# Kernel tuning notes

Measured on AMD Instinct MI355X. Metric: run time of the kernel, lower is better.

The kernel has to match this reference:

```python
import jax, jax.numpy as jnp
import numpy as np

NEG = 0.01  # leaky_relu negative slope used throughout AttentiveFP


def _seg_softmax(logits, seg, num):
    # softmax over entries grouped by segment id (PyG softmax w/ 1e-16 eps)
    m = jax.ops.segment_max(logits, seg, num_segments=num)
    m = jnp.where(jnp.isfinite(m), m, 0.0)
    e = jnp.exp(logits - m[seg])
    s = jax.ops.segment_sum(e, seg, num_segments=num)
    return e / (s[seg] + 1e-16)


def _gru(x, h, wi, wh, bi, bh):
    # torch.nn.GRUCell math
    gi = x @ wi.T + bi
    gh = h @ wh.T + bh
    ir, iz, inn = jnp.split(gi, 3, axis=-1)
    hr, hz, hn = jnp.split(gh, 3, axis=-1)
    r = jax.nn.sigmoid(ir + hr)
    z = jax.nn.sigmoid(iz + hz)
    n = jnp.tanh(inn + r * hn)
    return (1.0 - z) * n + z * h


def _forward(x, edge_attr, mol_feats, lin1_w, lin1_b, gate_lin1_w, gate_lin2_w, gate_att_l, gate_att_r, gate_bias, grus_wi, grus_wh, grus_bi, grus_bh, atom_w, atom_att_src, atom_att_dst, atom_bias, mol_w, mol_att_src, mol_att_dst, mol_bias, lin2_w, lin2_b, fcm0_w, fcm0_b, fcm1_w, fcm1_b, fcm2_w, fcm2_b, fc0_w, fc0_b, fc1_w, fc1_b, fc2_w, fc2_b, fc3_w, fc3_b, fc4_w, fc4_b, edge_index, batch):
    N = x.shape[0]
    G = mol_feats.shape[0]
    src, dst = edge_index[0], edge_index[1]
    lrelu = lambda v: jax.nn.leaky_relu(v, NEG)
    # AttentiveFP (eval mode: dropout off)
    xh = lrelu(x @ lin1_w.T + lin1_b)  # [N,H]
    # --- GATEConv: edge-conditioned attention, add aggregation ---
    m = lrelu(jnp.concatenate([xh[src], edge_attr], axis=-1) @ gate_lin1_w.T)  # [E,H]
    a = lrelu(m @ gate_att_l + (xh @ gate_att_r)[dst])
    a = _seg_softmax(a, dst, N)
    h = jax.ops.segment_sum((m @ gate_lin2_w.T) * a[:, None], dst, num_segments=N) + gate_bias
    xh = jax.nn.relu(_gru(jax.nn.elu(h), xh, grus_wi[0], grus_wh[0], grus_bi[0], grus_bh[0]))
    # --- GATConv layers (num_layers-1 = 2, heads=1, no self loops) ---
    for l in range(2):
        xl = xh @ atom_w[l].T
        a = lrelu((xl @ atom_att_src[l])[src] + (xl @ atom_att_dst[l])[dst])
        a = _seg_softmax(a, dst, N)
        h = jax.ops.segment_sum(xl[src] * a[:, None], dst, num_segments=N) + atom_bias[l]
        xh = jax.nn.relu(_gru(jax.nn.elu(h), xh, grus_wi[1 + l], grus_wh[1 + l], grus_bi[1 + l], grus_bh[1 + l]))
    # --- attentive graph readout (num_timesteps = 3) ---
    out = jax.nn.relu(jax.ops.segment_sum(xh, batch, num_segments=G))  # [G,H]
    xm = xh @ mol_w.T            # atom-side lin (x fixed across timesteps)
    a_src = xm @ mol_att_src
    for _ in range(3):
        a = lrelu(a_src + ((out @ mol_w.T) @ mol_att_dst)[batch])
        a = _seg_softmax(a, batch, G)
        h = jax.ops.segment_sum(xm * a[:, None], batch, num_segments=G) + mol_bias
        out = jax.nn.relu(_gru(jax.nn.elu(h), out, grus_wi[3], grus_wh[3], grus_bi[3], grus_bh[3]))
    hg = out @ lin2_w.T + lin2_b  # [G,256]
    # --- mol-feature MLP branch (SiLU) ---
    hm = jax.nn.silu(mol_feats @ fcm0_w.T + fcm0_b)
    hm = jax.nn.silu(hm @ fcm1_w.T + fcm1_b)
    hm = jax.nn.silu(hm @ fcm2_w.T + fcm2_b)
    # --- fusion MLP ---
    hg = jnp.concatenate([hg, hm], axis=1)  # [G,512]
    hg = jax.nn.silu(hg @ fc0_w.T + fc0_b)
    hg = jax.nn.silu(hg @ fc1_w.T + fc1_b)
    hg = jax.nn.silu(hg @ fc2_w.T + fc2_b)
    hg = jax.nn.silu(hg @ fc3_w.T + fc3_b)
    return hg @ fc4_w.T + fc4_b  # [G,1]


def setup_inputs() -> dict:
    key = jax.random.key(0)
    ks = iter(jax.random.split(key, 64))
    def W(*shape):
        return jax.random.normal(next(ks), shape, jnp.float32) / np.float32(np.sqrt(shape[-1]))
    def B(*shape):
        return 0.02 * jax.random.normal(next(ks), shape, jnp.float32)
    N, E, G = 131072, 262144, 8192
    Fn, Fe, Fm, H = 64, 16, 200, 256
    return dict(
        x=jax.random.normal(next(ks), (N, Fn), jnp.float32),
        edge_attr=jax.random.normal(next(ks), (E, Fe), jnp.float32),
        mol_feats=jax.random.normal(next(ks), (G, Fm), jnp.float32),
        lin1_w=W(H, Fn), lin1_b=B(H),
        gate_lin1_w=W(H, H + Fe), gate_lin2_w=W(H, H),
        gate_att_l=W(H), gate_att_r=W(H), gate_bias=B(H),
        grus_wi=W(4, 3 * H, H), grus_wh=W(4, 3 * H, H), grus_bi=B(4, 3 * H), grus_bh=B(4, 3 * H),
        atom_w=W(2, H, H), atom_att_src=W(2, H), atom_att_dst=W(2, H), atom_bias=B(2, H),
        mol_w=W(H, H), mol_att_src=W(H), mol_att_dst=W(H), mol_bias=B(H),
        lin2_w=W(H, H), lin2_b=B(H),
        fcm0_w=W(H, Fm), fcm0_b=B(H), fcm1_w=W(H, H), fcm1_b=B(H), fcm2_w=W(H, H), fcm2_b=B(H),
        fc0_w=W(512, 512), fc0_b=B(512), fc1_w=W(512, 512), fc1_b=B(512),
        fc2_w=W(512, 512), fc2_b=B(512), fc3_w=W(128, 512), fc3_b=B(128),
        fc4_w=W(1, 128), fc4_b=B(1),
        edge_index=jax.random.randint(next(ks), (2, E), 0, N),
        batch=jnp.sort(jax.random.randint(next(ks), (N,), 0, G)),
    )


def reference(x, edge_attr, mol_feats, lin1_w, lin1_b, gate_lin1_w, gate_lin2_w, gate_att_l, gate_att_r, gate_bias, grus_wi, grus_wh, grus_bi, grus_bh, atom_w, atom_att_src, atom_att_dst, atom_bias, mol_w, mol_att_src, mol_att_dst, mol_bias, lin2_w, lin2_b, fcm0_w, fcm0_b, fcm1_w, fcm1_b, fcm2_w, fcm2_b, fc0_w, fc0_b, fc1_w, fc1_b, fc2_w, fc2_b, fc3_w, fc3_b, fc4_w, fc4_b, edge_index, batch):
    return _forward(x, edge_attr, mol_feats, lin1_w, lin1_b, gate_lin1_w, gate_lin2_w, gate_att_l, gate_att_r, gate_bias, grus_wi, grus_wh, grus_bi, grus_bh, atom_w, atom_att_src, atom_att_dst, atom_bias, mol_w, mol_att_src, mol_att_dst, mol_bias, lin2_w, lin2_b, fcm0_w, fcm0_b, fcm1_w, fcm1_b, fcm2_w, fcm2_b, fc0_w, fc0_b, fc1_w, fc1_b, fc2_w, fc2_b, fc3_w, fc3_b, fc4_w, fc4_b, edge_index, batch)
```

## Files before the change

kernel.cpp:

```cpp
#include <hip/hip_runtime.h>
#include <hip/hip_bf16.h>
#include <math.h>


typedef unsigned short u16;
typedef u16 u16x8 __attribute__((ext_vector_type(8)));
typedef short s16x8 __attribute__((ext_vector_type(8)));
typedef float f32x4 __attribute__((ext_vector_type(4)));

__device__ __forceinline__ float u2f(u16 u) { return __uint_as_float(((unsigned)u) << 16); }
__device__ __forceinline__ u16 f2u(float f) {
    return __builtin_bit_cast(u16, __float2bfloat16(f));
}

#define NEGS 0.01f

__device__ __forceinline__ unsigned fkey(float f) {
    unsigned u = __float_as_uint(f);
    return (u & 0x80000000u) ? ~u : (u | 0x80000000u);
}
__device__ __forceinline__ float funkey(unsigned k) {
    return (k & 0x80000000u) ? __uint_as_float(k ^ 0x80000000u) : __uint_as_float(~k);
}
#define KEY_NEG_INF 0x007FFFFFu

static inline int cdiv(int a, int b) { return (a + b - 1) / b; }

__global__ void fill_f32(float* p, float v, size_t n) {
    size_t i = (size_t)blockIdx.x * 256 + threadIdx.x;
    if (i < n) p[i] = v;
}
__global__ void fill_u32(unsigned* p, unsigned v, int n) {
    int i = blockIdx.x * 256 + threadIdx.x;
    if (i < n) p[i] = v;
}
__global__ void relu_inplace(float* p, size_t n) {
    size_t i = (size_t)blockIdx.x * 256 + threadIdx.x;
    if (i < n) p[i] = fmaxf(p[i], 0.f);
}
__global__ void copy_f2b(const float* s, u16* d, size_t n) {
    size_t i = (size_t)blockIdx.x * 256 + threadIdx.x;
    if (i < n) d[i] = f2u(s[i]);
}
__global__ void copy_ff(const float* s, float* d, size_t n) {
    size_t i = (size_t)blockIdx.x * 256 + threadIdx.x;
    if (i < n) d[i] = s[i];
}
__global__ void matvecT_k(const float* W, const float* a, float* v, int K, int Jout) {
    int j = blockIdx.x * 256 + threadIdx.x;
    if (j >= Jout) return;
    float s = 0.f;
    for (int k = 0; k < K; k++) s += W[(size_t)k * Jout + j] * a[k];
    v[j] = s;
}
__global__ void edge_add_lrelu(float* elog, const float* r, const int* dsti, int E) {
    int i = blockIdx.x * 256 + threadIdx.x;
    if (i < E) {
        float v = elog[i] + r[dsti[i]];
        elog[i] = v > 0.f ? v : NEGS * v;
    }
}
__global__ void pair_logit(float* elog, const float* s, const float* d,
                           const int* srci, const int* dsti, int E) {
    int i = blockIdx.x * 256 + threadIdx.x;
    if (i < E) {
        float v = s[srci[i]] + d[dsti[i]];
        elog[i] = v > 0.f ? v : NEGS * v;
    }
}
__global__ void node_logit(float* nlog, const float* asrc, const float* wg,
                           const int* batch, int N) {
    int i = blockIdx.x * 256 + threadIdx.x;
    if (i < N) {
        float v = asrc[i] + wg[batch[i]];
        nlog[i] = v > 0.f ? v : NEGS * v;
    }
}
__global__ void seg_max_k(const float* logit, const int* idx, unsigned* key, int n) {
    int i = blockIdx.x * 256 + threadIdx.x;
    if (i < n) atomicMax(&key[idx[i]], fkey(logit[i]));
}
__global__ void seg_exp_k(const float* logit, const int* idx, const unsigned* key,
                          float* ex, float* sum, int n) {
    int i = blockIdx.x * 256 + threadIdx.x;
    if (i < n) {
        float e = expf(logit[i] - funkey(key[idx[i]]));
        ex[i] = e;
        atomicAdd(&sum[idx[i]], e);
    }
}
__global__ void seg_div_k(const float* ex, const int* idx, const float* sum,
                          float* a, int n) {
    int i = blockIdx.x * 256 + threadIdx.x;
    if (i < n) a[i] = ex[i] / (sum[idx[i]] + 1e-16f);
}
__global__ void scatter_rows_b(const u16* V, const int* gsrc, const float* sc,
                               const int* gdst, float* dst, int M) {
    int r = blockIdx.x;
    if (r >= M) return;
    int c = threadIdx.x;
    int vr = gsrc ? gsrc[r] : r;
    float v = u2f(V[(size_t)vr * 256 + c]);
    if (sc) v *= sc[r];
    atomicAdd(&dst[(size_t)gdst[r] * 256 + c], v);
}
__global__ void rowdot2_b(const u16* X, const float* v1, const float* v2,
                          float* o1, float* o2, int M) {
    int r = blockIdx.x * 4 + (threadIdx.x >> 6);
    int lane = threadIdx.x & 63;
    if (r >= M) return;
    const u16* row = X + (size_t)r * 256 + lane * 4;
    float p1 = 0.f, p2 = 0.f;
#pragma unroll
    for (int q = 0; q < 4; q++) {
        float xv = u2f(row[q]);
        p1 += xv * v1[lane * 4 + q];
        if (v2) p2 += xv * v2[lane * 4 + q];
    }
    for (int off = 32; off; off >>= 1) {
        p1 += __shfl_down(p1, off);
        if (v2) p2 += __shfl_down(p2, off);
    }
    if (lane == 0) {
        o1[r] = p1;
        if (v2) o2[r] = p2;
    }
}
__global__ void rowdot_f(const float* X, const float* v1, float* o1, int M) {
    int r = blockIdx.x * 4 + (threadIdx.x >> 6);
    int lane = threadIdx.x & 63;
    if (r >= M) return;
    float4 a = ((const float4*)(X + (size_t)r * 256))[lane];
    float4 b = ((const float4*)v1)[lane];
    float p1 = a.x * b.x + a.y * b.y + a.z * b.z + a.w * b.w;
    for (int off = 32; off; off >>= 1) p1 += __shfl_down(p1, off);
    if (lane == 0) o1[r] = p1;
}
__global__ void fc4_k(const float* X, const float* w, const float* b, float* out, int G) {
    int g = blockIdx.x * 4 + (threadIdx.x >> 6);
    int lane = threadIdx.x & 63;
    if (g >= G) return;
    float2 xv = ((const float2*)(X + (size_t)g * 128))[lane];
    float2 wv = ((const float2*)w)[lane];
    float p = xv.x * wv.x + xv.y * wv.y;
    for (int off = 32; off; off >>= 1) p += __shfl_down(p, off);
    if (lane == 0) out[g] = p + b[0];
}

__global__ void pack_w(const float* s1, const float* s2, int K1, int Ksrc,
                       int Nout, int Kp, u16* dst) {
    int idx = blockIdx.x * 256 + threadIdx.x;
    int kiters = Kp >> 5;
    int total = (Nout >> 7) * kiters * 512;
    if (idx >= total) return;
    int c = idx & 511;
    int rest = idx >> 9;
    int ki = rest % kiters, nb = rest / kiters;
    int n = (nb << 7) + (((c >> 6) & 7) << 4) + (c & 15);
    int k0 = (ki << 5) + (((c >> 4) & 3) << 3);
    u16x8 vh, vl;
#pragma unroll
    for (int j = 0; j < 8; j++) {
        int k = k0 + j;
        float f = 0.f;
        if (k < K1) f = s1[(size_t)n * K1 + k];
        else if (k < Ksrc) f = s2[(size_t)n * (Ksrc - K1) + (k - K1)];
        u16 h = f2u(f);
        vh[j] = h;
        vl[j] = f2u(f - u2f(h));
    }
    ((u16x8*)dst)[idx] = vh;
    ((u16x8*)dst)[idx + total] = vl;
}
__global__ void pack_gru_w(const float* wi, const float* wh, u16* dst) {
    int idx = blockIdx.x * 256 + threadIdx.x;
    const int total = 8 * 16 * 512;
    if (idx >= total) return;
    int c = idx & 511, rest = idx >> 9;
    int ki = rest & 15, nb = rest >> 4;
    int n = (nb << 7) + (((c >> 6) & 7) << 4) + (c & 15);
    int k0 = (ki << 5) + (((c >> 4) & 3) << 3);
    int grp = n >> 6, sub = (n >> 4) & 3, ch = grp * 16 + (n & 15);
    u16x8 vh, vl;
#pragma unroll
    for (int j = 0; j < 8; j++) {
        int k = k0 + j;
        float f;
        if (sub < 3) {
            int srow = sub * 256 + ch;
            f = (k < 256) ? wi[(size_t)srow * 256 + k]
                          : wh[(size_t)srow * 256 + (k - 256)];
        } else {
            f = (k < 256) ? 0.f : wh[(size_t)(512 + ch) * 256 + (k - 256)];
        }
        u16 h = f2u(f);
        vh[j] = h;
        vl[j] = f2u(f - u2f(h));
    }
    ((u16x8*)dst)[idx] = vh;
    ((u16x8*)dst)[idx + total] = vl;
}
__global__ void pack_gru_b(const float* bi, const float* bh, float* bp) {
    int n = blockIdx.x * 256 + threadIdx.x;
    if (n >= 1024) return;
    int grp = n >> 6, sub = (n >> 4) & 3, ch = grp * 16 + (n & 15);
    float v;
    if (sub == 0) v = bi[ch] + bh[ch];
    else if (sub == 1) v = bi[256 + ch] + bh[256 + ch];
    else if (sub == 2) v = bi[512 + ch] + bh[512 + ch];
    else v = bh[512 + ch];
    bp[n] = v;
}

struct p8 { u16x8 hi, lo; };
__device__ __forceinline__ u16x8 zero8() {
    u16x8 z;
#pragma unroll
    for (int j = 0; j < 8; j++) z[j] = 0;
    return z;
}
__device__ __forceinline__ p8 sp_zero() { p8 r; r.hi = zero8(); r.lo = zero8(); return r; }
__device__ __forceinline__ p8 sp_b(const u16* p) {
    p8 r;
    r.hi = *(const u16x8*)p;
    r.lo = zero8();
    return r;
}
__device__ __forceinline__ p8 sp_f(const float* p) {
    p8 r;
#pragma unroll
    for (int j = 0; j < 8; j++) {
        float x = p[j];
        u16 h = f2u(x);
        r.hi[j] = h;
        r.lo[j] = f2u(x - u2f(h));
    }
    return r;
}
__device__ __forceinline__ p8 sp_eluf(const float* p) {
    p8 r;
#pragma unroll
    for (int j = 0; j < 8; j++) {
        float x = p[j];
        float e = x > 0.f ? x : expm1f(x);
        u16 h = f2u(e);
        r.hi[j] = h;
        r.lo[j] = f2u(e - u2f(h));
    }
    return r;
}
template <int ALD>
__device__ __forceinline__ p8 ldA(bool valid, int k, int Ksrc, const u16* ab,
                                  const float* af, const float* x2) {
    if (!valid) return sp_zero();
    if (ALD == 1) {
        if (k >= Ksrc) return sp_zero();
        return sp_f(af + k);
    }
    if (ALD == 2) {
        if (k < 256) return sp_b(ab + k);
        if (k < 272) return sp_f(x2 + (k - 256));
        return sp_zero();
    }
    if (ALD == 3) {
        if (k < 256) return sp_eluf(af + k);
        return sp_b(ab + (k - 256));
    }
    if (k < 256) return sp_eluf(af + k);
    return sp_f(x2 + (k - 256));
}
template <int ALD>
__device__ __forceinline__ bool lo_zero(int ki) {
    if (ALD == 2) return ki < 8;
    if (ALD == 3) return ki >= 8;
    return false;
}
template <int ACT>
__device__ __forceinline__ float actf(float v) {
    if (ACT == 1) return v > 0.f ? v : NEGS * v;
    if (ACT == 3) return v / (1.f + expf(-v));
    return v;
}

template <int ALD, int ACT, int EPI>
__global__ __launch_bounds__(256, 2) void mgemm(
    int M, int Kp, int Ksrc,
    const float* Af, int lda, const u16* Ab,
    const int* gidx, const float* X2f, const u16* Wp,
    const float* b1,
    float* Cf, u16* Cb, int ldc,
    const float* attv, float* dotout,
    const int* didx, const float* escale, float* scat) {
    __shared__ u16x8 lsAh[512];
    __shared__ u16x8 lsAl[512];
    __shared__ u16x8 lsWh[512];
    __shared__ u16x8 lsWl[512];
    const int t = threadIdx.x;
    const int m0 = blockIdx.x * 128;
    const int nb = blockIdx.y;
    const int kiters = Kp >> 5;
    const int r0 = ((t >> 6) << 4) | (t & 15);
    const int kq = ((t >> 4) & 3) << 3;
    const int mA[2] = {m0 + r0, m0 + r0 + 64};
    const u16* abr[2];
    const float* afr[2];
    const float* x2r[2];
    bool val[2];
#pragma unroll
    for (int h = 0; h < 2; h++) {
        int m = mA[h];
        val[h] = (m < M);
        int ms = val[h] ? m : 0;
        abr[h] = nullptr; afr[h] = nullptr; x2r[h] = nullptr;
        if (ALD == 1) {
            afr[h] = Af + (size_t)ms * lda;
        } else if (ALD == 2) {
            abr[h] = Ab + (size_t)gidx[ms] * 256;
            x2r[h] = X2f + (size_t)ms * 16;
        } else if (ALD == 3) {
            afr[h] = Af + (size_t)ms * 256;
            abr[h] = Ab + (size_t)ms * 256;
        } else {
            afr[h] = Af + (size_t)ms * 256;
            x2r[h] = X2f + (size_t)ms * 256;
        }
    }
    const int wave = t >> 6, lane = t & 63;
    const int wm = (wave >> 1) << 6, wn = (wave & 1) << 6;
    f32x4 acc[4][4];
#pragma unroll
    for (int i = 0; i < 4; i++)
#pragma unroll
        for (int j = 0; j < 4; j++) {
            acc[i][j][0] = 0.f; acc[i][j][1] = 0.f; acc[i][j][2] = 0.f; acc[i][j][3] = 0.f;
        }
    const u16x8* wh0 = (const u16x8*)Wp + ((size_t)nb * kiters << 9);
    const u16x8* wl0 = wh0 + ((size_t)gridDim.y * kiters << 9);
    for (int ki = 0; ki < kiters; ki++) {
        int kb = (ki << 5) + kq;
        p8 a0 = ldA<ALD>(val[0], kb, Ksrc, abr[0], afr[0], x2r[0]);
        p8 a1 = ldA<ALD>(val[1], kb, Ksrc, abr[1], afr[1], x2r[1]);
        lsAh[t] = a0.hi; lsAl[t] = a0.lo;
        lsAh[t + 256] = a1.hi; lsAl[t + 256] = a1.lo;
        const u16x8* wsh = wh0 + ((size_t)ki << 9);
        const u16x8* wsl = wl0 + ((size_t)ki << 9);
        lsWh[t] = wsh[t]; lsWh[t + 256] = wsh[t + 256];
        lsWl[t] = wsl[t]; lsWl[t + 256] = wsl[t + 256];
        __syncthreads();
        s16x8 ah[4], al[4], wh[4], wl[4];
#pragma unroll
        for (int f = 0; f < 4; f++) {
            int ai = ((wm >> 4) + f) * 64 + lane;
            int wi = ((wn >> 4) + f) * 64 + lane;
            ah[f] = __builtin_bit_cast(s16x8, lsAh[ai]);
            al[f] = __builtin_bit_cast(s16x8, lsAl[ai]);
            wh[f] = __builtin_bit_cast(s16x8, lsWh[wi]);
            wl[f] = __builtin_bit_cast(s16x8, lsWl[wi]);
        }
        bool skip_lh = lo_zero<ALD>(ki);
#pragma unroll
        for (int fi = 0; fi < 4; fi++)
#pragma unroll
            for (int fj = 0; fj < 4; fj++) {
                acc[fi][fj] = __builtin_amdgcn_mfma_f32_16x16x32_bf16(
                    ah[fi], wh[fj], acc[fi][fj], 0, 0, 0);
                if (!skip_lh)
                    acc[fi][fj] = __builtin_amdgcn_mfma_f32_16x16x32_bf16(
                        al[fi], wh[fj], acc[fi][fj], 0, 0, 0);
                acc[fi][fj] = __builtin_amdgcn_mfma_f32_16x16x32_bf16(
                    ah[fi], wl[fj], acc[fi][fj], 0, 0, 0);
            }
        __syncthreads();
    }
    const int col = lane & 15, quad = lane >> 4;
    const int n_base = nb * 128 + wn;
    if (EPI == 2) {
        float dp[4][4] = {};
#pragma unroll
        for (int fi = 0; fi < 4; fi++)
#pragma unroll
            for (int fj = 0; fj < 4; fj++) {
                int nn = n_base + fj * 16 + col;
                float av = attv[nn];
#pragma unroll
                for (int r = 0; r < 4; r++) dp[fi][r] += actf<ACT>(acc[fi][fj][r]) * av;
            }
#pragma unroll
        for (int fi = 0; fi < 4; fi++)
#pragma unroll
            for (int r = 0; r < 4; r++) {
                float p = dp[fi][r];
                p += __shfl_down(p, 8);
                p += __shfl_down(p, 4);
                p += __shfl_down(p, 2);
                p += __shfl_down(p, 1);
                int mm = m0 + wm + fi * 16 + quad * 4 + r;
                if (col == 0 && mm < M) atomicAdd(dotout + mm, p);
            }
    } else if (EPI == 3) {
#pragma unroll
        for (int fi = 0; fi < 4; fi++)
#pragma unroll
            for (int r = 0; r < 4; r++) {
                int mm = m0 + wm + fi * 16 + quad * 4 + r;
                if (mm >= M) continue;
                int d = didx[mm];
                float s = escale[mm];
                float* rowp = scat + (size_t)d * 256;
#pragma unroll
                for (int fj = 0; fj < 4; fj++) {
                    int nn = n_base + fj * 16 + col;
                    atomicAdd(rowp + nn, actf<ACT>(acc[fi][fj][r]) * s);
                }
            }
    } else {
#pragma unroll
        for (int fj = 0; fj < 4; fj++) {
            int nn = n_base + fj * 16 + col;
            float bb = b1 ? b1[nn] : 0.f;
#pragma unroll
            for (int fi = 0; fi < 4; fi++)
#pragma unroll
                for (int r = 0; r < 4; r++) {
                    int mm = m0 + wm + fi * 16 + quad * 4 + r;
                    if (mm >= M) continue;
                    float v = actf<ACT>(acc[fi][fj][r] + bb);
                    if (EPI == 1) Cb[(size_t)mm * ldc + nn] = f2u(v);
                    else Cf[(size_t)mm * ldc + nn] = v;
                }
        }
    }
}

template <int ALD, bool HB>
__global__ __launch_bounds__(256, 2) void mgemm_gru(
    int M,
    const float* Af, const u16* Ab, const float* X2f,
    const u16* Wp, const float* bp,
    const u16* hb, const float* hf, float* of) {
    __shared__ u16x8 lsAh[512];
    __shared__ u16x8 lsAl[512];
    __shared__ u16x8 lsWh[512];
    __shared__ u16x8 lsWl[512];
    const int t = threadIdx.x;
    const int m0 = blockIdx.x * 128;
    const int nb = blockIdx.y;
    const int r0 = ((t >> 6) << 4) | (t & 15);
    const int kq = ((t >> 4) & 3) << 3;
    const int mA[2] = {m0 + r0, m0 + r0 + 64};
    const u16* abr[2];
    const float* afr[2];
    const float* x2r[2];
    bool val[2];
#pragma unroll
    for (int h = 0; h < 2; h++) {
        int m = mA[h];
        val[h] = (m < M);
        int ms = val[h] ? m : 0;
        abr[h] = nullptr; x2r[h] = nullptr;
        afr[h] = Af + (size_t)ms * 256;
        if (ALD == 3) abr[h] = Ab + (size_t)ms * 256;
        else x2r[h] = X2f + (size_t)ms * 256;
    }
    const int wave = t >> 6, lane = t & 63;
    const int wm = (wave >> 1) << 6, wn = (wave & 1) << 6;
    f32x4 acc[4][4];
#pragma unroll
    for (int i = 0; i < 4; i++)
#pragma unroll
        for (int j = 0; j < 4; j++) {
            acc[i][j][0] = 0.f; acc[i][j][1] = 0.f; acc[i][j][2] = 0.f; acc[i][j][3] = 0.f;
        }
    const u16x8* wh0 = (const u16x8*)Wp + ((size_t)nb * 16 << 9);
    const u16x8* wl0 = (const u16x8*)Wp + (size_t)(8 * 16 * 512) + ((size_t)nb * 16 << 9);
    for (int ki = 0; ki < 16; ki++) {
        int kb = (ki << 5) + kq;
        p8 a0 = ldA<ALD>(val[0], kb, 512, abr[0], afr[0], x2r[0]);
        p8 a1 = ldA<ALD>(val[1], kb, 512, abr[1], afr[1], x2r[1]);
        lsAh[t] = a0.hi; lsAl[t] = a0.lo;
        lsAh[t + 256] = a1.hi; lsAl[t + 256] = a1.lo;
        const u16x8* wsh = wh0 + ((size_t)ki << 9);
        const u16x8* wsl = wl0 + ((size_t)ki << 9);
        lsWh[t] = wsh[t]; lsWh[t + 256] = wsh[t + 256];
        lsWl[t] = wsl[t]; lsWl[t + 256] = wsl[t + 256];
        __syncthreads();
        s16x8 ah[4], al[4], wh[4], wl[4];
#pragma unroll
        for (int f = 0; f < 4; f++) {
            int ai = ((wm >> 4) + f) * 64 + lane;
            int wi = ((wn >> 4) + f) * 64 + lane;
            ah[f] = __builtin_bit_cast(s16x8, lsAh[ai]);
            al[f] = __builtin_bit_cast(s16x8, lsAl[ai]);
            wh[f] = __builtin_bit_cast(s16x8, lsWh[wi]);
            wl[f] = __builtin_bit_cast(s16x8, lsWl[wi]);
        }
        bool skip_lh = lo_zero<ALD>(ki);
        bool hn_zero = (ki < 8);
#pragma unroll
        for (int fi = 0; fi < 4; fi++)
#pragma unroll
            for (int fj = 0; fj < 4; fj++) {
                if (fj == 3 && hn_zero) continue;
                acc[fi][fj] = __builtin_amdgcn_mfma_f32_16x16x32_bf16(
                    ah[fi], wh[fj], acc[fi][fj], 0, 0, 0);
                if (!skip_lh)
                    acc[fi][fj] = __builtin_amdgcn_mfma_f32_16x16x32_bf16(
                        al[fi], wh[fj], acc[fi][fj], 0, 0, 0);
                acc[fi][fj] = __builtin_amdgcn_mfma_f32_16x16x32_bf16(
                    ah[fi], wl[fj], acc[fi][fj], 0, 0, 0);
            }
        __syncthreads();
    }
    const int col = lane & 15, quad = lane >> 4;
    const int nbase = nb * 128 + wn;
    float br = bp[nbase + col];
    float bz = bp[nbase + 16 + col];
    float bn = bp[nbase + 32 + col];
    float bhn = bp[nbase + 48 + col];
    int ch = (nb * 2 + (wn >> 6)) * 16 + col;
#pragma unroll
    for (int fi = 0; fi < 4; fi++)
#pragma unroll
        for (int r = 0; r < 4; r++) {
            int m = m0 + wm + fi * 16 + quad * 4 + r;
            if (m >= M) continue;
            float rs = acc[fi][0][r] + br;
            float zs = acc[fi][1][r] + bz;
            float nsv = acc[fi][2][r] + bn;
            float hnv = acc[fi][3][r] + bhn;
            float rr = 1.f / (1.f + expf(-rs));
            float zz = 1.f / (1.f + expf(-zs));
            float nn = tanhf(nsv - hnv + rr * hnv);
            float ho = HB ? u2f(hb[(size_t)m * 256 + ch]) : hf[(size_t)m * 256 + ch];
            of[(size_t)m * 256 + ch] = fmaxf((1.f - zz) * nn + zz * ho, 0.f);
        }
}

extern "C" void kernel_launch(void* const* d_in, const int* in_sizes, int n_in,
                              void* d_out, int out_size, void* d_ws, size_t ws_size,
                              hipStream_t stream) {
    const float* x = (const float*)d_in[0];
    const float* edge_attr = (const float*)d_in[1];
    const float* mol_feats = (const float*)d_in[2];
    const float* lin1_w = (const float*)d_in[3];
    const float* lin1_b = (const float*)d_in[4];
    const float* gate_lin1_w = (const float*)d_in[5];
    const float* gate_lin2_w = (const float*)d_in[6];
    const float* gate_att_l = (const float*)d_in[7];
    const float* gate_att_r = (const float*)d_in[8];
    const float* gate_bias = (const float*)d_in[9];
    const float* grus_wi = (const float*)d_in[10];
    const float* grus_wh = (const float*)d_in[11];
    const float* grus_bi = (const float*)d_in[12];
    const float* grus_bh = (const float*)d_in[13];
    const float* atom_w = (const float*)d_in[14];
    const float* atom_att_src = (const float*)d_in[15];
    const float* atom_att_dst = (const float*)d_in[16];
    const float* atom_bias = (const float*)d_in[17];
    const float* mol_w = (const float*)d_in[18];
    const float* mol_att_src = (const float*)d_in[19];
    const float* mol_att_dst = (const float*)d_in[20];
    const float* mol_bias = (const float*)d_in[21];
    const float* lin2_w = (const float*)d_in[22];
    const float* lin2_b = (const float*)d_in[23];
    const float* fcm0_w = (const float*)d_in[24];
    const float* fcm0_b = (const float*)d_in[25];
    const float* fcm1_w = (const float*)d_in[26];
    const float* fcm1_b = (const float*)d_in[27];
    const float* fcm2_w = (const float*)d_in[28];
    const float* fcm2_b = (const float*)d_in[29];
    const float* fc0_w = (const float*)d_in[30];
    const float* fc0_b = (const float*)d_in[31];
    const float* fc1_w = (const float*)d_in[32];
    const float* fc1_b = (const float*)d_in[33];
    const float* fc2_w = (const float*)d_in[34];
    const float* fc2_b = (const float*)d_in[35];
    const float* fc3_w = (const float*)d_in[36];
    const float* fc3_b = (const float*)d_in[37];
    const float* fc4_w = (const float*)d_in[38];
    const float* fc4_b = (const float*)d_in[39];
    const int* edge_index = (const int*)d_in[40];
    const int* batch = (const int*)d_in[41];
    float* out_final = (float*)d_out;

    const int N = in_sizes[0] / 64;
    const int E = in_sizes[1] / 16;
    const int G = in_sizes[2] / 200;
    const int* srcE = edge_index;
    const int* dstE = edge_index + E;

    char* base = (char*)d_ws;
    size_t off = 0;
    auto alloc = [&](size_t bytes) -> char* {
        char* p = base + off;
        off += (bytes + 255) & ~(size_t)255;
        return p;
    };
    u16* xh = (u16*)alloc((size_t)N * 256 * 2);
    float* hagg = (float*)alloc((size_t)N * 256 * 4);
    float* outg = (float*)alloc((size_t)G * 256 * 4);
    float* hgr = (float*)alloc((size_t)G * 256 * 4);
    float* elog = (float*)alloc((size_t)E * 4);
    float* eexp = (float*)alloc((size_t)E * 4);
    float* aedge = (float*)alloc((size_t)E * 4);
    unsigned* nkey = (unsigned*)alloc((size_t)N * 4);
    float* nsum = (float*)alloc((size_t)N * 4);
    float* ns1 = (float*)alloc((size_t)N * 4);
    float* ns2 = (float*)alloc((size_t)N * 4);
    unsigned* gkey = (unsigned*)alloc((size_t)G * 4);
    float* gsum = (float*)alloc((size_t)G * 4);
    float* wgb = (float*)alloc((size_t)G * 4);
    float* vbuf = (float*)alloc(1024 * 4);
    u16* pk_lin1 = (u16*)alloc(256 * 64 * 2 * 2);
    u16* pk_g1 = (u16*)alloc(256 * 288 * 2 * 2);
    u16* pk_g2 = (u16*)alloc(256 * 256 * 2 * 2);
    u16* pk_gruF[4];
    float* bp_gru[4];
    for (int l = 0; l < 4; l++) {
        pk_gruF[l] = (u16*)alloc(1024 * 512 * 2 * 2);
        bp_gru[l] = (float*)alloc(1024 * 4);
    }
    u16* pk_atom[2];
    for (int l = 0; l < 2; l++) pk_atom[l] = (u16*)alloc(256 * 256 * 2 * 2);
    u16* pk_mol = (u16*)alloc(256 * 256 * 2 * 2);
    u16* pk_lin2 = (u16*)alloc(256 * 256 * 2 * 2);
    u16* pk_fcm0 = (u16*)alloc(256 * 224 * 2 * 2);
    u16* pk_fcm1 = (u16*)alloc(256 * 256 * 2 * 2);
    u16* pk_fcm2 = (u16*)alloc(256 * 256 * 2 * 2);
    u16* pk_fc0 = (u16*)alloc(512 * 512 * 2 * 2);
    u16* pk_fc1 = (u16*)alloc(512 * 512 * 2 * 2);
    u16* pk_fc2 = (u16*)alloc(512 * 512 * 2 * 2);
    u16* pk_fc3 = (u16*)alloc(128 * 512 * 2 * 2);
    size_t fixed_bytes = off;
    if (fixed_bytes + (size_t)2 * 1024 * 1024 > ws_size) {
        fill_f32<<<cdiv(out_size, 256), 256, 0, stream>>>(out_final, (float)ws_size,
                                                          (size_t)out_size);
        return;
    }
    size_t avail = ws_size - fixed_bytes;
    float* cbuf = (float*)(base + fixed_bytes);
    int Mc = (int)((avail / 1024) & ~(size_t)127);
    if (Mc > N) Mc = N;
    if (Mc < 128) Mc = 128;
    float* fbufA = hagg;
    float* fbufB = fbufA + (size_t)G * 512;
    float* fbufC = fbufB + (size_t)G * 512;
    float* f128 = fbufC + (size_t)G * 512;
    float* hm1 = f128 + (size_t)G * 128;
    float* hm2 = hm1 + (size_t)G * 256;

    auto pack = [&](const float* s1, const float* s2, int K1, int Ksrc, int Nout,
                    int Kp, u16* dst) {
        int total = (Nout >> 7) * (Kp >> 5) * 512;
        pack_w<<<cdiv(total, 256), 256, 0, stream>>>(s1, s2, K1, Ksrc, Nout, Kp, dst);
    };
    pack(lin1_w, nullptr, 64, 64, 256, 64, pk_lin1);
    pack(gate_lin1_w, nullptr, 272, 272, 256, 288, pk_g1);
    pack(gate_lin2_w, nullptr, 256, 256, 256, 256, pk_g2);
    for (int l = 0; l < 4; l++) {
        pack_gru_w<<<cdiv(8 * 16 * 512, 256), 256, 0, stream>>>(
            grus_wi + (size_t)l * 768 * 256, grus_wh + (size_t)l * 768 * 256,
            pk_gruF[l]);
        pack_gru_b<<<4, 256, 0, stream>>>(grus_bi + (size_t)l * 768,
                                          grus_bh + (size_t)l * 768, bp_gru[l]);
    }
    for (int l = 0; l < 2; l++)
        pack(atom_w + (size_t)l * 256 * 256, nullptr, 256, 256, 256, 256, pk_atom[l]);
    pack(mol_w, nullptr, 256, 256, 256, 256, pk_mol);
    pack(lin2_w, nullptr, 256, 256, 256, 256, pk_lin2);
    pack(fcm0_w, nullptr, 200, 200, 256, 224, pk_fcm0);
    pack(fcm1_w, nullptr, 256, 256, 256, 256, pk_fcm1);
    pack(fcm2_w, nullptr, 256, 256, 256, 256, pk_fcm2);
    pack(fc0_w, nullptr, 512, 512, 512, 512, pk_fc0);
    pack(fc1_w, nullptr, 512, 512, 512, 512, pk_fc1);
    pack(fc2_w, nullptr, 512, 512, 512, 512, pk_fc2);
    pack(fc3_w, nullptr, 512, 512, 128, 512, pk_fc3);

#define NIL nullptr, nullptr, nullptr, nullptr, nullptr

    auto node_gru = [&](int l, const u16* Wpre, const float* bpre) {
        for (int c0 = 0; c0 < N; c0 += Mc) {
            int Ms = N - c0 < Mc ? N - c0 : Mc;
            int gx = cdiv(Ms, 128);
            mgemm<1, 0, 0><<<dim3(gx, 2), 256, 0, stream>>>(Ms, 256, 256,
                hagg + (size_t)c0 * 256, 256, nullptr, nullptr, nullptr,
                Wpre, bpre, cbuf, nullptr, 256, NIL);
            mgemm_gru<3, true><<<dim3(gx, 8), 256, 0, stream>>>(Ms,
                cbuf, xh + (size_t)c0 * 256, nullptr, pk_gruF[l], bp_gru[l],
                xh + (size_t)c0 * 256, nullptr, hagg + (size_t)c0 * 256);
        }
        copy_f2b<<<(int)(((size_t)N * 256 + 255) / 256), 256, 0, stream>>>(
            hagg, xh, (size_t)N * 256);
    };

    mgemm<1, 1, 1><<<dim3(cdiv(N, 128), 2), 256, 0, stream>>>(N, 64, 64,
        x, 64, nullptr, nullptr, nullptr, pk_lin1, lin1_b,
        nullptr, xh, 256, NIL);

    fill_f32<<<cdiv(E, 256), 256, 0, stream>>>(elog, 0.f, (size_t)E);
    mgemm<2, 1, 2><<<dim3(cdiv(E, 128), 2), 256, 0, stream>>>(E, 288, 272,
        nullptr, 0, xh, srcE, edge_attr, pk_g1, nullptr,
        nullptr, nullptr, 0, gate_att_l, elog, nullptr, nullptr, nullptr);
    rowdot2_b<<<cdiv(N, 4), 256, 0, stream>>>(xh, gate_att_r, nullptr, ns1, nullptr, N);
    edge_add_lrelu<<<cdiv(E, 256), 256, 0, stream>>>(elog, ns1, dstE, E);
    fill_u32<<<cdiv(N, 256), 256, 0, stream>>>(nkey, KEY_NEG_INF, N);
    fill_f32<<<cdiv(N, 256), 256, 0, stream>>>(nsum, 0.f, (size_t)N);
    seg_max_k<<<cdiv(E, 256), 256, 0, stream>>>(elog, dstE, nkey, E);
    seg_exp_k<<<cdiv(E, 256), 256, 0, stream>>>(elog, dstE, nkey, eexp, nsum, E);
    seg_div_k<<<cdiv(E, 256), 256, 0, stream>>>(eexp, dstE, nsum, aedge, E);
    fill_f32<<<(int)(((size_t)N * 256 + 255) / 256), 256, 0, stream>>>(
        hagg, 0.f, (size_t)N * 256);
    mgemm<2, 1, 3><<<dim3(cdiv(E, 128), 2), 256, 0, stream>>>(E, 288, 272,
        nullptr, 0, xh, srcE, edge_attr, pk_g1, nullptr,
        nullptr, nullptr, 0, nullptr, nullptr, dstE, aedge, hagg);
    node_gru(0, pk_g2, gate_bias);

    for (int l = 0; l < 2; l++) {
        const float* aw = atom_w + (size_t)l * 256 * 256;
        matvecT_k<<<1, 256, 0, stream>>>(aw, atom_att_src + (size_t)l * 256, vbuf, 256, 256);
        matvecT_k<<<1, 256, 0, stream>>>(aw, atom_att_dst + (size_t)l * 256, vbuf + 256, 256, 256);
        rowdot2_b<<<cdiv(N, 4), 256, 0, stream>>>(xh, vbuf, vbuf + 256, ns1, ns2, N);
        pair_logit<<<cdiv(E, 256), 256, 0, stream>>>(elog, ns1, ns2, srcE, dstE, E);
        fill_u32<<<cdiv(N, 256), 256, 0, stream>>>(nkey, KEY_NEG_INF, N);
        fill_f32<<<cdiv(N, 256), 256, 0, stream>>>(nsum, 0.f, (size_t)N);
        seg_max_k<<<cdiv(E, 256), 256, 0, stream>>>(elog, dstE, nkey, E);
        seg_exp_k<<<cdiv(E, 256), 256, 0, stream>>>(elog, dstE, nkey, eexp, nsum, E);
        seg_div_k<<<cdiv(E, 256), 256, 0, stream>>>(eexp, dstE, nsum, aedge, E);
        fill_f32<<<(int)(((size_t)N * 256 + 255) / 256), 256, 0, stream>>>(
            hagg, 0.f, (size_t)N * 256);
        scatter_rows_b<<<E, 256, 0, stream>>>(xh, srcE, aedge, dstE, hagg, E);
        node_gru(1 + l, pk_atom[l], atom_bias + (size_t)l * 256);
    }

    fill_f32<<<(int)(((size_t)G * 256 + 255) / 256), 256, 0, stream>>>(
        outg, 0.f, (size_t)G * 256);
    scatter_rows_b<<<N, 256, 0, stream>>>(xh, nullptr, nullptr, batch, outg, N);
    relu_inplace<<<(int)(((size_t)G * 256 + 255) / 256), 256, 0, stream>>>(
        outg, (size_t)G * 256);
    matvecT_k<<<1, 256, 0, stream>>>(mol_w, mol_att_dst, vbuf, 256, 256);
    matvecT_k<<<1, 256, 0, stream>>>(mol_w, mol_att_src, vbuf + 256, 256, 256);
    rowdot2_b<<<cdiv(N, 4), 256, 0, stream>>>(xh, vbuf + 256, nullptr, ns1, nullptr, N);
    int McG = Mc < G ? Mc : G;
    for (int t = 0; t < 3; t++) {
        rowdot_f<<<cdiv(G, 4), 256, 0, stream>>>(outg, vbuf, wgb, G);
        node_logit<<<cdiv(N, 256), 256, 0, stream>>>(elog, ns1, wgb, batch, N);
        fill_u32<<<cdiv(G, 256), 256, 0, stream>>>(gkey, KEY_NEG_INF, G);
        fill_f32<<<cdiv(G, 256), 256, 0, stream>>>(gsum, 0.f, (size_t)G);
        seg_max_k<<<cdiv(N, 256), 256, 0, stream>>>(elog, batch, gkey, N);
        seg_exp_k<<<cdiv(N, 256), 256, 0, stream>>>(elog, batch, gkey, eexp, gsum, N);
        seg_div_k<<<cdiv(N, 256), 256, 0, stream>>>(eexp, batch, gsum, aedge, N);
        fill_f32<<<(int)(((size_t)G * 256 + 255) / 256), 256, 0, stream>>>(
            hgr, 0.f, (size_t)G * 256);
        scatter_rows_b<<<N, 256, 0, stream>>>(xh, nullptr, aedge, batch, hgr, N);
        for (int c0 = 0; c0 < G; c0 += McG) {
            int Ms = G - c0 < McG ? G - c0 : McG;
            int gx = cdiv(Ms, 128);
            mgemm<1, 0, 0><<<dim3(gx, 2), 256, 0, stream>>>(Ms, 256, 256,
                hgr + (size_t)c0 * 256, 256, nullptr, nullptr, nullptr,
                pk_mol, mol_bias, cbuf, nullptr, 256, NIL);
            mgemm_gru<4, false><<<dim3(gx, 8), 256, 0, stream>>>(Ms,
                cbuf, nullptr, outg + (size_t)c0 * 256, pk_gruF[3], bp_gru[3],
                nullptr, outg + (size_t)c0 * 256, hgr + (size_t)c0 * 256);
        }
        copy_ff<<<(int)(((size_t)G * 256 + 255) / 256), 256, 0, stream>>>(
            hgr, outg, (size_t)G * 256);
    }

    int gG = cdiv(G, 128);
    mgemm<1, 0, 0><<<dim3(gG, 2), 256, 0, stream>>>(G, 256, 256, outg, 256,
        nullptr, nullptr, nullptr, pk_lin2, lin2_b,
        fbufA, nullptr, 512, NIL);
    mgemm<1, 3, 0><<<dim3(gG, 2), 256, 0, stream>>>(G, 224, 200, mol_feats, 200,
        nullptr, nullptr, nullptr, pk_fcm0, fcm0_b,
        hm1, nullptr, 256, NIL);
    mgemm<1, 3, 0><<<dim3(gG, 2), 256, 0, stream>>>(G, 256, 256, hm1, 256,
        nullptr, nullptr, nullptr, pk_fcm1, fcm1_b,
        hm2, nullptr, 256, NIL);
    mgemm<1, 3, 0><<<dim3(gG, 2), 256, 0, stream>>>(G, 256, 256, hm2, 256,
        nullptr, nullptr, nullptr, pk_fcm2, fcm2_b,
        fbufA + 256, nullptr, 512, NIL);
    mgemm<1, 3, 0><<<dim3(gG, 4), 256, 0, stream>>>(G, 512, 512, fbufA, 512,
        nullptr, nullptr, nullptr, pk_fc0, fc0_b,
        fbufB, nullptr, 512, NIL);
    mgemm<1, 3, 0><<<dim3(gG, 4), 256, 0, stream>>>(G, 512, 512, fbufB, 512,
        nullptr, nullptr, nullptr, pk_fc1, fc1_b,
        fbufC, nullptr, 512, NIL);
    mgemm<1, 3, 0><<<dim3(gG, 4), 256, 0, stream>>>(G, 512, 512, fbufC, 512,
        nullptr, nullptr, nullptr, pk_fc2, fc2_b,
        fbufB, nullptr, 512, NIL);
    mgemm<1, 3, 0><<<dim3(gG, 1), 256, 0, stream>>>(G, 512, 512, fbufB, 512,
        nullptr, nullptr, nullptr, pk_fc3, fc3_b,
        f128, nullptr, 128, NIL);
    fc4_k<<<cdiv(G, 4), 256, 0, stream>>>(f128, fc4_w, fc4_b, out_final, G);
}
```

Before: 6.628 ms.

## Replace atomic scatter aggregation with CSR gather and sorted segment reductions

```diff
diff --git a/kernel.cpp b/kernel.cpp
--- a/kernel.cpp
+++ b/kernel.cpp
@@ -34,17 +34,9 @@
     int i = blockIdx.x * 256 + threadIdx.x;
     if (i < n) p[i] = v;
 }
-__global__ void relu_inplace(float* p, size_t n) {
-    size_t i = (size_t)blockIdx.x * 256 + threadIdx.x;
-    if (i < n) p[i] = fmaxf(p[i], 0.f);
-}
 __global__ void copy_f2b(const float* s, u16* d, size_t n) {
     size_t i = (size_t)blockIdx.x * 256 + threadIdx.x;
     if (i < n) d[i] = f2u(s[i]);
-}
-__global__ void copy_ff(const float* s, float* d, size_t n) {
-    size_t i = (size_t)blockIdx.x * 256 + threadIdx.x;
-    if (i < n) d[i] = s[i];
 }
 __global__ void matvecT_k(const float* W, const float* a, float* v, int K, int Jout) {
     int j = blockIdx.x * 256 + threadIdx.x;
@@ -93,16 +85,6 @@
                           float* a, int n) {
     int i = blockIdx.x * 256 + threadIdx.x;
     if (i < n) a[i] = ex[i] / (sum[idx[i]] + 1e-16f);
-}
-__global__ void scatter_rows_b(const u16* V, const int* gsrc, const float* sc,
-                               const int* gdst, float* dst, int M) {
-    int r = blockIdx.x;
-    if (r >= M) return;
-    int c = threadIdx.x;
-    int vr = gsrc ? gsrc[r] : r;
-    float v = u2f(V[(size_t)vr * 256 + c]);
-    if (sc) v *= sc[r];
-    atomicAdd(&dst[(size_t)gdst[r] * 256 + c], v);
 }
 __global__ void rowdot2_b(const u16* X, const float* v1, const float* v2,
                           float* o1, float* o2, int M) {
@@ -145,6 +127,63 @@
     float p = xv.x * wv.x + xv.y * wv.y;
     for (int off = 32; off; off >>= 1) p += __shfl_down(p, off);
     if (lane == 0) out[g] = p + b[0];
+}
+
+__global__ void count_dst(const int* dst, int* cnt, int E) {
+    int i = blockIdx.x * 256 + threadIdx.x;
+    if (i < E) atomicAdd(&cnt[dst[i]], 1);
+}
+__global__ void alloc_rows(const int* cnt, int* rowstart, int* cursor, int N) {
+    int i = blockIdx.x * 256 + threadIdx.x;
+    if (i < N) rowstart[i] = atomicAdd(cursor, cnt[i]);
+}
+__global__ void fill_csr(const int* dst, const int* rowstart, int* fillc,
+                         int* eorder, int E) {
+    int e = blockIdx.x * 256 + threadIdx.x;
+    if (e >= E) return;
+    int d = dst[e];
+    int s = rowstart[d] + atomicAdd(&fillc[d], 1);
+    eorder[s] = e;
+}
+template <int MODE>
+__global__ void csr_reduce(const int* rowstart, const int* cnt, const int* eorder,
+                           const float* a, const int* srcE, const u16* X,
+                           float* out, int N) {
+    int d = blockIdx.x;
+    if (d >= N) return;
+    int c = threadIdx.x;
+    int rs = rowstart[d], k = cnt[d];
+    float acc = 0.f;
+    for (int s = 0; s < k; s++) {
+        int e = eorder[rs + s];
+        float av = a[e];
+        const u16* row = (MODE == 0) ? X + (size_t)srcE[e] * 256 : X + (size_t)e * 256;
+        acc += av * u2f(row[c]);
+    }
+    out[(size_t)d * 256 + c] = acc;
+}
+__global__ void graph_bounds(const int* batch, int* gs, int* ge, int N) {
+    int i = blockIdx.x * 256 + threadIdx.x;
+    if (i >= N) return;
+    int b = batch[i];
+    atomicMin(&gs[b], i);
+    atomicMax(&ge[b], i + 1);
+}
+template <bool RELU>
+__global__ void seg_red(const int* gs, const int* ge, const u16* X, const float* sc,
+                        float* out, int G) {
+    int g = blockIdx.x;
+    if (g >= G) return;
+    int c = threadIdx.x;
+    int s = gs[g], e = ge[g];
+    float acc = 0.f;
+    if (s < e)
+        for (int i = s; i < e; i++) {
+            float v = u2f(X[(size_t)i * 256 + c]);
+            if (sc) v *= sc[i];
+            acc += v;
+        }
+    out[(size_t)g * 256 + c] = RELU ? fmaxf(acc, 0.f) : acc;
 }
 
 __global__ void pack_w(const float* s1, const float* s2, int K1, int Ksrc,
@@ -283,7 +322,7 @@
 }
 
 template <int ALD, int ACT, int EPI>
-__global__ __launch_bounds__(256, 2) void mgemm(
+__global__ __launch_bounds__(256, 4) void mgemm(
     int M, int Kp, int Ksrc,
     const float* Af, int lda, const u16* Ab,
     const int* gidx, const float* X2f, const u16* Wp,
@@ -383,7 +422,14 @@
                 int nn = n_base + fj * 16 + col;
                 float av = attv[nn];
 #pragma unroll
-                for (int r = 0; r < 4; r++) dp[fi][r] += actf<ACT>(acc[fi][fj][r]) * av;
+                for (int r = 0; r < 4; r++) {
+                    float v = actf<ACT>(acc[fi][fj][r]);
+                    dp[fi][r] += v * av;
+                    if (Cb) {
+                        int mm = m0 + wm + fi * 16 + quad * 4 + r;
+                        if (mm < M) Cb[(size_t)mm * ldc + nn] = f2u(v);
+                    }
+                }
             }
 #pragma unroll
         for (int fi = 0; fi < 4; fi++)
@@ -432,12 +478,12 @@
     }
 }
 
-template <int ALD, bool HB>
-__global__ __launch_bounds__(256, 2) void mgemm_gru(
+template <int ALD, bool HB, bool OB>
+__global__ __launch_bounds__(256, 4) void mgemm_gru(
     int M,
     const float* Af, const u16* Ab, const float* X2f,
     const u16* Wp, const float* bp,
-    const u16* hb, const float* hf, float* of) {
+    const u16* hb, const float* hf, float* of, u16* ob) {
     __shared__ u16x8 lsAh[512];
     __shared__ u16x8 lsAl[512];
     __shared__ u16x8 lsWh[512];
@@ -532,7 +578,9 @@
             float zz = 1.f / (1.f + expf(-zs));
             float nn = tanhf(nsv - hnv + rr * hnv);
             float ho = HB ? u2f(hb[(size_t)m * 256 + ch]) : hf[(size_t)m * 256 + ch];
-            of[(size_t)m * 256 + ch] = fmaxf((1.f - zz) * nn + zz * ho, 0.f);
+            float o = fmaxf((1.f - zz) * nn + zz * ho, 0.f);
+            if (OB) ob[(size_t)m * 256 + ch] = f2u(o);
+            else of[(size_t)m * 256 + ch] = o;
         }
 }
 
@@ -596,10 +644,10 @@
         off += (bytes + 255) & ~(size_t)255;
         return p;
     };
-    u16* xh = (u16*)alloc((size_t)N * 256 * 2);
+    u16* xhA = (u16*)alloc((size_t)N * 256 * 2);
     float* hagg = (float*)alloc((size_t)N * 256 * 4);
     float* outg = (float*)alloc((size_t)G * 256 * 4);
-    float* hgr = (float*)alloc((size_t)G * 256 * 4);
+    float* hgrb = (float*)alloc((size_t)G * 256 * 4);
     float* elog = (float*)alloc((size_t)E * 4);
     float* eexp = (float*)alloc((size_t)E * 4);
     float* aedge = (float*)alloc((size_t)E * 4);
@@ -611,6 +659,13 @@
     float* gsum = (float*)alloc((size_t)G * 4);
     float* wgb = (float*)alloc((size_t)G * 4);
     float* vbuf = (float*)alloc(1024 * 4);
+    int* ecnt = (int*)alloc((size_t)N * 4);
+    int* efill = (int*)alloc((size_t)N * 4);
+    int* erowst = (int*)alloc((size_t)N * 4);
+    int* eorder = (int*)alloc((size_t)E * 4);
+    int* cursor = (int*)alloc(256);
+    int* gs = (int*)alloc((size_t)G * 4);
+    int* ge = (int*)alloc((size_t)G * 4);
     u16* pk_lin1 = (u16*)alloc(256 * 64 * 2 * 2);
     u16* pk_g1 = (u16*)alloc(256 * 288 * 2 * 2);
     u16* pk_g2 = (u16*)alloc(256 * 256 * 2 * 2);
@@ -631,15 +686,24 @@
     u16* pk_fc1 = (u16*)alloc(512 * 512 * 2 * 2);
     u16* pk_fc2 = (u16*)alloc(512 * 512 * 2 * 2);
     u16* pk_fc3 = (u16*)alloc(128 * 512 * 2 * 2);
-    size_t fixed_bytes = off;
-    if (fixed_bytes + (size_t)2 * 1024 * 1024 > ws_size) {
+    size_t fixed_core = off;
+    if (fixed_core + (size_t)2 * 1024 * 1024 > ws_size) {
         fill_f32<<<cdiv(out_size, 256), 256, 0, stream>>>(out_final, (float)ws_size,
                                                           (size_t)out_size);
         return;
     }
-    size_t avail = ws_size - fixed_bytes;
-    float* cbuf = (float*)(base + fixed_bytes);
-    int Mc = (int)((avail / 1024) & ~(size_t)127);
+    u16* xhB = nullptr;
+    bool use_pp = false;
+    if (ws_size - off >= (size_t)N * 512 + (size_t)2 * 1024 * 1024) {
+        xhB = (u16*)alloc((size_t)N * 512);
+        use_pp = true;
+    }
+    size_t workbytes = ws_size - off;
+    char* workp = base + off;
+    float* cbuf = (float*)workp;
+    u16* mtmp = (u16*)workp;
+    bool use_mtmp = workbytes >= (size_t)E * 512;
+    int Mc = (int)((workbytes / 1024) & ~(size_t)127);
     if (Mc > N) Mc = N;
     if (Mc < 128) Mc = 128;
     float* fbufA = hagg;
@@ -676,7 +740,20 @@
     pack(fc2_w, nullptr, 512, 512, 512, 512, pk_fc2);
     pack(fc3_w, nullptr, 512, 512, 128, 512, pk_fc3);
 
+    fill_u32<<<cdiv(N, 256), 256, 0, stream>>>((unsigned*)ecnt, 0u, N);
+    fill_u32<<<cdiv(N, 256), 256, 0, stream>>>((unsigned*)efill, 0u, N);
+    fill_u32<<<1, 256, 0, stream>>>((unsigned*)cursor, 0u, 1);
+    count_dst<<<cdiv(E, 256), 256, 0, stream>>>(dstE, ecnt, E);
+    alloc_rows<<<cdiv(N, 256), 256, 0, stream>>>(ecnt, erowst, cursor, N);
+    fill_csr<<<cdiv(E, 256), 256, 0, stream>>>(dstE, erowst, efill, eorder, E);
+    fill_u32<<<cdiv(G, 256), 256, 0, stream>>>((unsigned*)gs, (unsigned)N, G);
+    fill_u32<<<cdiv(G, 256), 256, 0, stream>>>((unsigned*)ge, 0u, G);
+    graph_bounds<<<cdiv(N, 256), 256, 0, stream>>>(batch, gs, ge, N);
+
 #define NIL nullptr, nullptr, nullptr, nullptr, nullptr
+
+    u16* xh_cur = xhA;
+    u16* xh_nxt = xhB;
 
     auto node_gru = [&](int l, const u16* Wpre, const float* bpre) {
         for (int c0 = 0; c0 < N; c0 += Mc) {
@@ -685,89 +762,100 @@
             mgemm<1, 0, 0><<<dim3(gx, 2), 256, 0, stream>>>(Ms, 256, 256,
                 hagg + (size_t)c0 * 256, 256, nullptr, nullptr, nullptr,
                 Wpre, bpre, cbuf, nullptr, 256, NIL);
-            mgemm_gru<3, true><<<dim3(gx, 8), 256, 0, stream>>>(Ms,
-                cbuf, xh + (size_t)c0 * 256, nullptr, pk_gruF[l], bp_gru[l],
-                xh + (size_t)c0 * 256, nullptr, hagg + (size_t)c0 * 256);
-        }
-        copy_f2b<<<(int)(((size_t)N * 256 + 255) / 256), 256, 0, stream>>>(
-            hagg, xh, (size_t)N * 256);
+            if (use_pp)
+                mgemm_gru<3, true, true><<<dim3(gx, 8), 256, 0, stream>>>(Ms,
+                    cbuf, xh_cur + (size_t)c0 * 256, nullptr, pk_gruF[l], bp_gru[l],
+                    xh_cur + (size_t)c0 * 256, nullptr, nullptr,
+                    xh_nxt + (size_t)c0 * 256);
+            else
+                mgemm_gru<3, true, false><<<dim3(gx, 8), 256, 0, stream>>>(Ms,
+                    cbuf, xh_cur + (size_t)c0 * 256, nullptr, pk_gruF[l], bp_gru[l],
+                    xh_cur + (size_t)c0 * 256, nullptr,
+                    hagg + (size_t)c0 * 256, nullptr);
+        }
+        if (use_pp) {
+            u16* t2 = xh_cur; xh_cur = xh_nxt; xh_nxt = t2;
+        } else {
+            copy_f2b<<<(int)(((size_t)N * 256 + 255) / 256), 256, 0, stream>>>(
+                hagg, xh_cur, (size_t)N * 256);
+        }
     };
 
     mgemm<1, 1, 1><<<dim3(cdiv(N, 128), 2), 256, 0, stream>>>(N, 64, 64,
         x, 64, nullptr, nullptr, nullptr, pk_lin1, lin1_b,
-        nullptr, xh, 256, NIL);
+        nullptr, xh_cur, 256, NIL);
 
     fill_f32<<<cdiv(E, 256), 256, 0, stream>>>(elog, 0.f, (size_t)E);
     mgemm<2, 1, 2><<<dim3(cdiv(E, 128), 2), 256, 0, stream>>>(E, 288, 272,
-        nullptr, 0, xh, srcE, edge_attr, pk_g1, nullptr,
-        nullptr, nullptr, 0, gate_att_l, elog, nullptr, nullptr, nullptr);
-    rowdot2_b<<<cdiv(N, 4), 256, 0, stream>>>(xh, gate_att_r, nullptr, ns1, nullptr, N);
+        nullptr, 0, xh_cur, srcE, edge_attr, pk_g1, nullptr,
+        nullptr, use_mtmp ? mtmp : nullptr, 256,
+        gate_att_l, elog, nullptr, nullptr, nullptr);
+    rowdot2_b<<<cdiv(N, 4), 256, 0, stream>>>(xh_cur, gate_att_r, nullptr, ns1, nullptr, N);
     edge_add_lrelu<<<cdiv(E, 256), 256, 0, stream>>>(elog, ns1, dstE, E);
     fill_u32<<<cdiv(N, 256), 256, 0, stream>>>(nkey, KEY_NEG_INF, N);
     fill_f32<<<cdiv(N, 256), 256, 0, stream>>>(nsum, 0.f, (size_t)N);
     seg_max_k<<<cdiv(E, 256), 256, 0, stream>>>(elog, dstE, nkey, E);
     seg_exp_k<<<cdiv(E, 256), 256, 0, stream>>>(elog, dstE, nkey, eexp, nsum, E);
     seg_div_k<<<cdiv(E, 256), 256, 0, stream>>>(eexp, dstE, nsum, aedge, E);
-    fill_f32<<<(int)(((size_t)N * 256 + 255) / 256), 256, 0, stream>>>(
-        hagg, 0.f, (size_t)N * 256);
-    mgemm<2, 1, 3><<<dim3(cdiv(E, 128), 2), 256, 0, stream>>>(E, 288, 272,
-        nullptr, 0, xh, srcE, edge_attr, pk_g1, nullptr,
-        nullptr, nullptr, 0, nullptr, nullptr, dstE, aedge, hagg);
+    if (use_mtmp) {
+        csr_reduce<1><<<N, 256, 0, stream>>>(erowst, ecnt, eorder, aedge, nullptr,
+                                             mtmp, hagg, N);
+    } else {
+        fill_f32<<<(int)(((size_t)N * 256 + 255) / 256), 256, 0, stream>>>(
+            hagg, 0.f, (size_t)N * 256);
+        mgemm<2, 1, 3><<<dim3(cdiv(E, 128), 2), 256, 0, stream>>>(E, 288, 272,
+            nullptr, 0, xh_cur, srcE, edge_attr, pk_g1, nullptr,
+            nullptr, nullptr, 0, nullptr, nullptr, dstE, aedge, hagg);
+    }
     node_gru(0, pk_g2, gate_bias);
 
     for (int l = 0; l < 2; l++) {
         const float* aw = atom_w + (size_t)l * 256 * 256;
         matvecT_k<<<1, 256, 0, stream>>>(aw, atom_att_src + (size_t)l * 256, vbuf, 256, 256);
         matvecT_k<<<1, 256, 0, stream>>>(aw, atom_att_dst + (size_t)l * 256, vbuf + 256, 256, 256);
-        rowdot2_b<<<cdiv(N, 4), 256, 0, stream>>>(xh, vbuf, vbuf + 256, ns1, ns2, N);
+        rowdot2_b<<<cdiv(N, 4), 256, 0, stream>>>(xh_cur, vbuf, vbuf + 256, ns1, ns2, N);
         pair_logit<<<cdiv(E, 256), 256, 0, stream>>>(elog, ns1, ns2, srcE, dstE, E);
         fill_u32<<<cdiv(N, 256), 256, 0, stream>>>(nkey, KEY_NEG_INF, N);
         fill_f32<<<cdiv(N, 256), 256, 0, stream>>>(nsum, 0.f, (size_t)N);
         seg_max_k<<<cdiv(E, 256), 256, 0, stream>>>(elog, dstE, nkey, E);
         seg_exp_k<<<cdiv(E, 256), 256, 0, stream>>>(elog, dstE, nkey, eexp, nsum, E);
         seg_div_k<<<cdiv(E, 256), 256, 0, stream>>>(eexp, dstE, nsum, aedge, E);
-        fill_f32<<<(int)(((size_t)N * 256 + 255) / 256), 256, 0, stream>>>(
-            hagg, 0.f, (size_t)N * 256);
-        scatter_rows_b<<<E, 256, 0, stream>>>(xh, srcE, aedge, dstE, hagg, E);
+        csr_reduce<0><<<N, 256, 0, stream>>>(erowst, ecnt, eorder, aedge, srcE,
+                                             xh_cur, hagg, N);
         node_gru(1 + l, pk_atom[l], atom_bias + (size_t)l * 256);
     }
 
-    fill_f32<<<(int)(((size_t)G * 256 + 255) / 256), 256, 0, stream>>>(
-        outg, 0.f, (size_t)G * 256);
-    scatter_rows_b<<<N, 256, 0, stream>>>(xh, nullptr, nullptr, batch, outg, N);
-    relu_inplace<<<(int)(((size_t)G * 256 + 255) / 256), 256, 0, stream>>>(
-        outg, (size_t)G * 256);
+    seg_red<true><<<G, 256, 0, stream>>>(gs, ge, xh_cur, nullptr, outg, G);
     matvecT_k<<<1, 256, 0, stream>>>(mol_w, mol_att_dst, vbuf, 256, 256);
     matvecT_k<<<1, 256, 0, stream>>>(mol_w, mol_att_src, vbuf + 256, 256, 256);
-    rowdot2_b<<<cdiv(N, 4), 256, 0, stream>>>(xh, vbuf + 256, nullptr, ns1, nullptr, N);
+    rowdot2_b<<<cdiv(N, 4), 256, 0, stream>>>(xh_cur, vbuf + 256, nullptr, ns1, nullptr, N);
+    float* ogc = outg;
+    float* ogn = hgrb;
     int McG = Mc < G ? Mc : G;
     for (int t = 0; t < 3; t++) {
-        rowdot_f<<<cdiv(G, 4), 256, 0, stream>>>(outg, vbuf, wgb, G);
+        rowdot_f<<<cdiv(G, 4), 256, 0, stream>>>(ogc, vbuf, wgb, G);
         node_logit<<<cdiv(N, 256), 256, 0, stream>>>(elog, ns1, wgb, batch, N);
         fill_u32<<<cdiv(G, 256), 256, 0, stream>>>(gkey, KEY_NEG_INF, G);
         fill_f32<<<cdiv(G, 256), 256, 0, stream>>>(gsum, 0.f, (size_t)G);
         seg_max_k<<<cdiv(N, 256), 256, 0, stream>>>(elog, batch, gkey, N);
         seg_exp_k<<<cdiv(N, 256), 256, 0, stream>>>(elog, batch, gkey, eexp, gsum, N);
         seg_div_k<<<cdiv(N, 256), 256, 0, stream>>>(eexp, batch, gsum, aedge, N);
-        fill_f32<<<(int)(((size_t)G * 256 + 255) / 256), 256, 0, stream>>>(
-            hgr, 0.f, (size_t)G * 256);
-        scatter_rows_b<<<N, 256, 0, stream>>>(xh, nullptr, aedge, batch, hgr, N);
+        seg_red<false><<<G, 256, 0, stream>>>(gs, ge, xh_cur, aedge, ogn, G);
         for (int c0 = 0; c0 < G; c0 += McG) {
             int Ms = G - c0 < McG ? G - c0 : McG;
             int gx = cdiv(Ms, 128);
             mgemm<1, 0, 0><<<dim3(gx, 2), 256, 0, stream>>>(Ms, 256, 256,
-                hgr + (size_t)c0 * 256, 256, nullptr, nullptr, nullptr,
+                ogn + (size_t)c0 * 256, 256, nullptr, nullptr, nullptr,
                 pk_mol, mol_bias, cbuf, nullptr, 256, NIL);
-            mgemm_gru<4, false><<<dim3(gx, 8), 256, 0, stream>>>(Ms,
-                cbuf, nullptr, outg + (size_t)c0 * 256, pk_gruF[3], bp_gru[3],
-                nullptr, outg + (size_t)c0 * 256, hgr + (size_t)c0 * 256);
-        }
-        copy_ff<<<(int)(((size_t)G * 256 + 255) / 256), 256, 0, stream>>>(
-            hgr, outg, (size_t)G * 256);
+            mgemm_gru<4, false, false><<<dim3(gx, 8), 256, 0, stream>>>(Ms,
+                cbuf, nullptr, ogc + (size_t)c0 * 256, pk_gruF[3], bp_gru[3],
+                nullptr, ogc + (size_t)c0 * 256, ogn + (size_t)c0 * 256, nullptr);
+        }
+        float* tt = ogc; ogc = ogn; ogn = tt;
     }
 
     int gG = cdiv(G, 128);
-    mgemm<1, 0, 0><<<dim3(gG, 2), 256, 0, stream>>>(G, 256, 256, outg, 256,
+    mgemm<1, 0, 0><<<dim3(gG, 2), 256, 0, stream>>>(G, 256, 256, ogc, 256,
         nullptr, nullptr, nullptr, pk_lin2, lin2_b,
         fbufA, nullptr, 512, NIL);
     mgemm<1, 3, 0><<<dim3(gG, 2), 256, 0, stream>>>(G, 224, 200, mol_feats, 200,
```

Measured after the change: 6.257 ms. -5.6%, faster.
